# Performance work log

Hardware: AMD Instinct MI355X
Metric: run time of the kernel (lower is better)

Reference implementation:

```python
import jax, jax.numpy as jnp
import numpy as np
import math

B, C_IN, S, E, H, DFF = 8, 16, 1024, 128, 8, 512
DH = E // H
EPS_BN = 1e-5
EPS_LN = 1e-5


def _tape_pe(d_model, seq_len):
    pos = jnp.arange(seq_len, dtype=jnp.float32)[:, None]
    div = jnp.exp(jnp.arange(0, d_model, 2, dtype=jnp.float32) * (-math.log(10000.0) / d_model))
    ang = pos * div * (d_model / seq_len)
    pe = jnp.zeros((seq_len, d_model), dtype=jnp.float32)
    pe = pe.at[:, 0::2].set(jnp.sin(ang))
    pe = pe.at[:, 1::2].set(jnp.cos(ang))
    return pe  # [S, E]


def _ln(x, g, b, eps=EPS_LN):
    m = jnp.mean(x, axis=-1, keepdims=True)
    v = jnp.mean((x - m) ** 2, axis=-1, keepdims=True)
    return (x - m) / jnp.sqrt(v + eps) * g + b


def _bn(x, g, b, mean, var, eps=EPS_BN):
    # eval-mode BatchNorm2d over channel axis 1 of NCHW
    sh = (1, -1, 1, 1)
    return (x - mean.reshape(sh)) / jnp.sqrt(var.reshape(sh) + eps) * g.reshape(sh) + b.reshape(sh)


def setup_inputs() -> dict:
    key = jax.random.key(0)
    ks = jax.random.split(key, 24)
    f = lambda k, shape, s=0.05: (jax.random.normal(k, shape, dtype=jnp.float32) * s)
    inp = {
        'x': jax.random.normal(ks[0], (B, C_IN, S), dtype=jnp.float32),
        'conv1_w': f(ks[1], (E * 4, 1, 1, 7)),
        'conv1_b': f(ks[2], (E * 4,)),
        'bn1_g': 1.0 + f(ks[3], (E * 4,)),
        'bn1_b': f(ks[4], (E * 4,)),
        'bn1_m': jnp.zeros((E * 4,), jnp.float32),
        'bn1_v': jnp.ones((E * 4,), jnp.float32),
        'conv2_w': f(ks[5], (E, E * 4, C_IN, 1)),
        'conv2_b': f(ks[6], (E,)),
        'bn2_g': 1.0 + f(ks[7], (E,)),
        'bn2_b': f(ks[8], (E,)),
        'bn2_m': jnp.zeros((E,), jnp.float32),
        'bn2_v': jnp.ones((E,), jnp.float32),
        'wq': f(ks[9], (E, E)),
        'wk': f(ks[10], (E, E)),
        'wv': f(ks[11], (E, E)),
        'rel_bias_table': f(ks[12], (2 * S - 1, H), 0.02),
        'ln_attn_g': jnp.ones((E,), jnp.float32),
        'ln_attn_b': jnp.zeros((E,), jnp.float32),
        'ln1_g': jnp.ones((E,), jnp.float32),
        'ln1_b': jnp.zeros((E,), jnp.float32),
        'ln2_g': jnp.ones((E,), jnp.float32),
        'ln2_b': jnp.zeros((E,), jnp.float32),
        'ff_w1': f(ks[13], (DFF, E)),
        'ff_b1': f(ks[14], (DFF,)),
        'ff_w2': f(ks[15], (E, DFF)),
        'ff_b2': f(ks[16], (E,)),
    }
    return inp


def reference(x, conv1_w, conv1_b, bn1_g, bn1_b, bn1_m, bn1_v,
              conv2_w, conv2_b, bn2_g, bn2_b, bn2_m, bn2_v,
              wq, wk, wv, rel_bias_table,
              ln_attn_g, ln_attn_b, ln1_g, ln1_b, ln2_g, ln2_b,
              ff_w1, ff_b1, ff_w2, ff_b2):
    dn = ('NCHW', 'OIHW', 'NCHW')
    # conv stem: x [B, C_in, S] -> [B, 1, C_in, S]
    h = x[:, None, :, :]
    h = jax.lax.conv_general_dilated(h, conv1_w, (1, 1), [(0, 0), (3, 3)], dimension_numbers=dn)
    h = h + conv1_b[None, :, None, None]
    h = jax.nn.gelu(_bn(h, bn1_g, bn1_b, bn1_m, bn1_v), approximate=False)
    h = jax.lax.conv_general_dilated(h, conv2_w, (1, 1), [(0, 0), (0, 0)], dimension_numbers=dn)
    h = h + conv2_b[None, :, None, None]
    h = jax.nn.gelu(_bn(h, bn2_g, bn2_b, bn2_m, bn2_v), approximate=False)
    x_src = jnp.transpose(h[:, :, 0, :], (0, 2, 1))  # [B, S, E]

    # tAPE absolute positional encoding
    x_pos = x_src + _tape_pe(E, S)[None]

    # Attention_Rel_Scl (eRPE): bias added AFTER softmax, as in the original
    scale = E ** (-0.5)
    q = jnp.einsum('bsd,ed->bse', x_pos, wq).reshape(B, S, H, DH).transpose(0, 2, 1, 3)
    k = jnp.einsum('bsd,ed->bse', x_pos, wk).reshape(B, S, H, DH).transpose(0, 2, 1, 3)
    v = jnp.einsum('bsd,ed->bse', x_pos, wv).reshape(B, S, H, DH).transpose(0, 2, 1, 3)
    attn = jax.nn.softmax(jnp.einsum('bhid,bhjd->bhij', q, k) * scale, axis=-1)
    idx = jnp.arange(S)[:, None] - jnp.arange(S)[None, :] + (S - 1)  # [S, S]
    rel_bias = rel_bias_table[idx].transpose(2, 0, 1)[None]  # [1, H, S, S]
    attn = attn + rel_bias
    out = jnp.einsum('bhij,bhjd->bhid', attn, v).transpose(0, 2, 1, 3).reshape(B, S, E)
    out = _ln(out, ln_attn_g, ln_attn_b)

    att = _ln(x_src + out, ln1_g, ln1_b)
    ff = jnp.maximum(jnp.einsum('bsd,fd->bsf', att, ff_w1) + ff_b1, 0.0)
    ff = jnp.einsum('bsf,ef->bse', ff, ff_w2) + ff_b2
    y = _ln(att + ff, ln2_g, ln2_b)
    return jnp.transpose(y, (0, 2, 1))  # [B, E, S]
```

## Files before the change

### kernel.cpp

```cpp
#include <hip/hip_runtime.h>
#include <math.h>

#define BB    8
#define CIN   16
#define SS    1024
#define EE    128
#define HH    8
#define DHH   16
#define O1    512
#define DFFN  512
#define K2TOT 8192

#define PE_OFF    0
#define BN1SC_OFF 131072
#define BN1SH_OFF 131584
#define BN2SC_OFF 132096
#define BN2SH_OFF 132224
#define W1P_OFF   133120
#define WQKV_BF_OFF 135168
#define W1FF_BF_OFF 159744
#define W2FF_BF_OFF 192512
#define XSRC_OFF  262144
#define Q_OFF     1310720
#define KK_OFF    2359296
#define V_OFF     3407872
#define ATTN_OFF  4456448
#define ATT_OFF   5505024
#define FFH_OFF   6553600
#define W2CONV_BF_OFF 8650752

typedef __attribute__((ext_vector_type(8))) short short8;
typedef __attribute__((ext_vector_type(8))) unsigned short ushort8;
typedef __attribute__((ext_vector_type(4))) unsigned short us4;
typedef __attribute__((ext_vector_type(4))) float f32x4;
typedef _Float16 f16_t;
typedef __attribute__((ext_vector_type(4))) _Float16 half4;
typedef __attribute__((ext_vector_type(8))) _Float16 half8;

__device__ __forceinline__ float wave_sum(float v) {
    #pragma unroll
    for (int o = 32; o > 0; o >>= 1) v += __shfl_xor(v, o);
    return v;
}

__device__ __forceinline__ float gelu_exact(float x) {
    return 0.5f * x * (1.0f + erff(x * 0.7071067811865476f));
}

__device__ __forceinline__ float gelu_tanh(float x) {
    float x2 = x * x;
    float y = x * fmaf(0.0713548162f, x2, 1.5957691216f);
    float E = __expf(y);
    float r = __builtin_amdgcn_rcpf(E + 1.0f);
    return fmaf(-x, r, x);
}

__device__ __forceinline__ unsigned short f2bf(float f) {
    unsigned int u = __float_as_uint(f);
    unsigned int r = u + 0x7FFFu + ((u >> 16) & 1u);
    return (unsigned short)(r >> 16);
}

__device__ __forceinline__ float bf2f(unsigned short u) {
    return __uint_as_float(((unsigned int)u) << 16);
}

__device__ __forceinline__ void castw_body(const float* __restrict__ src,
                                           unsigned short* __restrict__ dst, int K, int tid) {
    int g = tid & 7, e = (tid >> 3) & 127, rest = tid >> 10;
    int KB = K >> 6;
    int kb = rest % KB, nb = rest / KB;
    int col = nb * 128 + e;
    const float* s = src + (size_t)col * K + kb * 64 + ((g ^ (e & 7)) << 3);
    ushort8 v;
    #pragma unroll
    for (int j = 0; j < 8; j++) v[j] = f2bf(s[j]);
    *(ushort8*)&dst[(size_t)tid << 3] = v;
}

__global__ __launch_bounds__(256) void k0_all(const float* __restrict__ conv1_w,
                                              const float* __restrict__ conv1_b,
                                              const float* __restrict__ bn1_g,
                                              const float* __restrict__ bn1_b,
                                              const float* __restrict__ bn1_m,
                                              const float* __restrict__ bn1_v,
                                              const float* __restrict__ conv2_w,
                                              const float* __restrict__ conv2_b,
                                              const float* __restrict__ bn2_g,
                                              const float* __restrict__ bn2_b,
                                              const float* __restrict__ bn2_m,
                                              const float* __restrict__ bn2_v,
                                              const float* __restrict__ wq,
                                              const float* __restrict__ wk,
                                              const float* __restrict__ wv,
                                              const float* __restrict__ ff_w1,
                                              const float* __restrict__ ff_w2,
                                              float* __restrict__ ws) {
    int bid = blockIdx.x, t = threadIdx.x;
    if (bid < 512) {
        int idx = bid * 256 + t;
        int s = idx >> 7, e = idx & 127;
        int i = e >> 1;
        float freq = expf((float)(2 * i) * (-9.210340371976184f / 128.0f));
        float ang = (float)s * freq * 0.125f;
        ws[PE_OFF + idx] = (e & 1) ? cosf(ang) : sinf(ang);
    } else if (bid < 515) {
        int u = (bid - 512) * 256 + t;
        if (u < 512) {
            float sc = bn1_g[u] * rsqrtf(bn1_v[u] + 1e-5f);
            ws[BN1SC_OFF + u] = sc;
            ws[BN1SH_OFF + u] = (conv1_b[u] - bn1_m[u]) * sc + bn1_b[u];
        } else if (u < 640) {
            int e = u - 512;
            float sc = bn2_g[e] * rsqrtf(bn2_v[e] + 1e-5f);
            ws[BN2SC_OFF + e] = sc;
            ws[BN2SH_OFF + e] = (conv2_b[e] - bn2_m[e]) * sc + bn2_b[e];
        }
    } else if (bid < 1027) {
        castw_body(conv2_w, (unsigned short*)(ws + W2CONV_BF_OFF), 8192, (bid - 515) * 256 + t);
    } else if (bid < 1035) {
        castw_body(wq, (unsigned short*)(ws + WQKV_BF_OFF), 128, (bid - 1027) * 256 + t);
    } else if (bid < 1043) {
        castw_body(wk, (unsigned short*)(ws + WQKV_BF_OFF) + 16384, 128, (bid - 1035) * 256 + t);
    } else if (bid < 1051) {
        castw_body(wv, (unsigned short*)(ws + WQKV_BF_OFF) + 32768, 128, (bid - 1043) * 256 + t);
    } else if (bid < 1083) {
        castw_body(ff_w1, (unsigned short*)(ws + W1FF_BF_OFF), 128, (bid - 1051) * 256 + t);
    } else if (bid < 1115) {
        castw_body(ff_w2, (unsigned short*)(ws + W2FF_BF_OFF), 512, (bid - 1083) * 256 + t);
    } else {
        unsigned short* w1p = (unsigned short*)(ws + W1P_OFF);
        for (int id = t; id < 4096; id += 256) {
            int o = id >> 3, u = id & 7;
            float sc = bn1_g[o] * rsqrtf(bn1_v[o] + 1e-5f);
            float v = (u < 7) ? conv1_w[o * 7 + u] * sc : 0.f;
            w1p[id] = f2bf(v);
        }
    }
}

__global__ __launch_bounds__(256) void k1_mfma(const float* __restrict__ x,
                                               float* __restrict__ ws) {
    __shared__ float xt[CIN][72];
    __shared__ unsigned short w1ps[128 * 8];
    __shared__ float sh1s[128];

    const int t = threadIdx.x;
    const int wave = t >> 6, lane = t & 63;
    const int row0 = blockIdx.x * 64;
    const int ksplit = blockIdx.y;
    const int b = row0 >> 10, s0 = row0 & 1023;
    const int obase = ksplit * 128;

    for (int i = t; i < CIN * 70; i += 256) {
        int c = i / 70, j = i % 70;
        int gs = s0 + j - 3;
        xt[c][j] = (gs >= 0 && gs < SS) ? x[(b * CIN + c) * SS + gs] : 0.f;
    }
    if (t < 128) {
        *(ushort8*)&w1ps[t << 3] =
            ((const ushort8*)((const unsigned short*)(ws + W1P_OFF)))[obase + t];
        sh1s[t] = ws[BN1SH_OFF + obase + t];
    }
    __syncthreads();

    const int lrow = lane & 15, lq = lane >> 4;
    const int srow_local = (wave << 4) + lrow;
    const int cbase = (lq & 1) << 3;

    float xv[56];
    #pragma unroll
    for (int c8 = 0; c8 < 8; ++c8)
        #pragma unroll
        for (int u = 0; u < 7; ++u)
            xv[c8 * 7 + u] = xt[cbase + c8][srow_local + u];

    int boff[16];
    #pragma unroll
    for (int ks2 = 0; ks2 < 2; ++ks2) {
        int G = (ks2 << 2) + lq;
        #pragma unroll
        for (int nf = 0; nf < 8; ++nf) {
            int e = (nf << 4) + lrow;
            boff[ks2 * 8 + nf] = (e << 7) + ((G ^ (e & 7)) << 4);
        }
    }

    const char* w2g = (const char*)(ws + W2CONV_BF_OFF);
    const int olq = lq >> 1;

    auto computeA = [&](int kbl, int ks2) -> short8 {
        int ol = (kbl << 2) + (ks2 << 1) + olq;
        ushort8 w8 = *(const ushort8*)&w1ps[ol << 3];
        float w0 = bf2f(w8[0]), w1_ = bf2f(w8[1]), w2_ = bf2f(w8[2]), w3 = bf2f(w8[3]);
        float w4 = bf2f(w8[4]), w5 = bf2f(w8[5]), w6 = bf2f(w8[6]);
        float sh = sh1s[ol];
        short8 a;
        #pragma unroll
        for (int j = 0; j < 8; ++j) {
            float p = xv[j*7]   * w0 + xv[j*7+1] * w1_ + xv[j*7+2] * w2_ + xv[j*7+3] * w3
                    + xv[j*7+4] * w4 + xv[j*7+5] * w5 + xv[j*7+6] * w6;
            a[j] = (short)f2bf(gelu_tanh(p + sh));
        }
        return a;
    };

    f32x4 acc[8];
    #pragma unroll
    for (int i = 0; i < 8; ++i) acc[i] = (f32x4){0.f, 0.f, 0.f, 0.f};

    #pragma unroll 1
    for (int kbl = 0; kbl < 32; ++kbl) {
        const char* g = w2g + ((size_t)((ksplit << 5) + kbl) << 14);
        short8 bA_[8];
        #pragma unroll
        for (int i = 0; i < 8; ++i) bA_[i] = *(const short8*)(g + boff[i]);
        short8 a0 = computeA(kbl, 0);
        short8 bB_[8];
        #pragma unroll
        for (int i = 0; i < 8; ++i) bB_[i] = *(const short8*)(g + boff[8 + i]);
        #pragma unroll
        for (int nf = 0; nf < 8; ++nf)
            acc[nf] = __builtin_amdgcn_mfma_f32_16x16x32_bf16(a0, bA_[nf], acc[nf], 0, 0, 0);
        short8 a1 = computeA(kbl, 1);
        #pragma unroll
        for (int nf = 0; nf < 8; ++nf)
            acc[nf] = __builtin_amdgcn_mfma_f32_16x16x32_bf16(a1, bB_[nf], acc[nf], 0, 0, 0);
    }

    float* P = ws + Q_OFF + (size_t)ksplit * 1048576;
    #pragma unroll
    for (int nf = 0; nf < 8; ++nf) {
        int e = (nf << 4) + lrow;
        #pragma unroll
        for (int r = 0; r < 4; ++r) {
            int srow = s0 + (wave << 4) + (lq << 2) + r;
            P[(((size_t)(b * SS + srow)) << 7) + e] = acc[nf][r];
        }
    }
}

__global__ __launch_bounds__(256) void k1b_combine(float* __restrict__ ws) {
    int f = (blockIdx.x * 256 + threadIdx.x) * 4;
    int e0 = f & 127;
    float4 p0 = *(const float4*)&ws[Q_OFF + f];
    float4 p1 = *(const float4*)&ws[KK_OFF + f];
    float4 p2 = *(const float4*)&ws[V_OFF + f];
    float4 p3 = *(const float4*)&ws[ATTN_OFF + f];
    float4 sc = *(const float4*)&ws[BN2SC_OFF + e0];
    float4 sh = *(const float4*)&ws[BN2SH_OFF + e0];
    float4 o;
    o.x = gelu_exact(fmaf((p0.x + p1.x) + (p2.x + p3.x), sc.x, sh.x));
    o.y = gelu_exact(fmaf((p0.y + p1.y) + (p2.y + p3.y), sc.y, sh.y));
    o.z = gelu_exact(fmaf((p0.z + p1.z) + (p2.z + p3.z), sc.z, sh.z));
    o.w = gelu_exact(fmaf((p0.w + p1.w) + (p2.w + p3.w), sc.w, sh.w));
    *(float4*)&ws[XSRC_OFF + f] = o;
}

__global__ __launch_bounds__(256) void k2_mfma(float* __restrict__ ws) {
    __shared__ unsigned short As[32 * 128];
    __shared__ unsigned short Bs[128 * 128];
    __shared__ float ys[32][132];
    const int t = threadIdx.x;
    const int rt = blockIdx.x, mat = blockIdx.y;
    const int wave = t >> 6, lane = t & 63;

    const char* bg = (const char*)((const unsigned short*)(ws + WQKV_BF_OFF) + mat * 16384);
    #pragma unroll
    for (int c8 = 0; c8 < 8; ++c8) {
        int off = c8 * 4096 + wave * 1024;
        __builtin_amdgcn_global_load_lds(
            (const __attribute__((address_space(1))) unsigned int*)(bg + off + lane * 16),
            (__attribute__((address_space(3))) unsigned int*)(&Bs[off >> 1]), 16, 0, 0);
    }
    const int bs0 = rt * 32;
    const int sl0 = bs0 & 1023;
    for (int i = t; i < 1024; i += 256) {
        int row = i >> 5, d0 = (i & 31) << 2;
        float4 xvv = *(const float4*)&ws[XSRC_OFF + (size_t)(bs0 + row) * EE + d0];
        float4 pv = *(const float4*)&ws[PE_OFF + (size_t)(sl0 + row) * EE + d0];
        us4 o;
        o[0] = f2bf(xvv.x + pv.x); o[1] = f2bf(xvv.y + pv.y);
        o[2] = f2bf(xvv.z + pv.z); o[3] = f2bf(xvv.w + pv.w);
        int slot = (d0 >> 3) ^ (row & 7);
        *(us4*)&As[(row << 7) + (slot << 3) + (d0 & 7)] = o;
    }
    __syncthreads();

    const int wr = wave >> 1, wc = wave & 1;
    const int lrow = lane & 15, lq = lane >> 4;
    f32x4 acc[4];
    #pragma unroll
    for (int i = 0; i < 4; i++) acc[i] = (f32x4){0.f, 0.f, 0.f, 0.f};

    #pragma unroll
    for (int ksname = 0; ksname < 4; ++ksname) {
        int G = (ksname << 2) + lq;
        int arow = (wr << 4) + lrow;
        short8 a = *(const short8*)&As[(arow << 7) + ((G ^ (arow & 7)) << 3)];
        #pragma unroll
        for (int nf = 0; nf < 4; ++nf) {
            int e = (wc << 6) + (nf << 4) + lrow;
            short8 bf = *(const short8*)&Bs[((G >> 3) << 13) + (e << 6) + (((G & 7) ^ (e & 7)) << 3)];
            acc[nf] = __builtin_amdgcn_mfma_f32_16x16x32_bf16(a, bf, acc[nf], 0, 0, 0);
        }
    }

    #pragma unroll
    for (int nf = 0; nf < 4; ++nf) {
        int e = (wc << 6) + (nf << 4) + lrow;
        #pragma unroll
        for (int r = 0; r < 4; ++r)
            ys[(wr << 4) + (lq << 2) + r][e] = acc[nf][r];
    }
    __syncthreads();

    const int b = bs0 >> 10;
    if (mat <= 1) {
        int row = t >> 3, h8 = t & 7;
        float scl = (mat == 0) ? 0.08838834764831845f : 1.0f;
        f16_t* dst = (f16_t*)(ws + (mat == 0 ? Q_OFF : KK_OFF))
                   + (((size_t)(b * HH + h8)) * SS + (sl0 + row)) * DHH;
        half8 v0, v1;
        #pragma unroll
        for (int d = 0; d < 8; d++) v0[d] = (f16_t)(ys[row][h8 * 16 + d] * scl);
        #pragma unroll
        for (int d = 0; d < 8; d++) v1[d] = (f16_t)(ys[row][h8 * 16 + 8 + d] * scl);
        *(half8*)&dst[0] = v0;
        *(half8*)&dst[8] = v1;
    } else {
        int c = t & 127, hf = t >> 7;
        int h8 = c >> 4, d2 = c & 15;
        f16_t* dst = (f16_t*)(ws + V_OFF)
                   + (((size_t)(b * HH + h8)) * DHH + d2) * SS + sl0 + hf * 16;
        half8 v0, v1;
        #pragma unroll
        for (int r = 0; r < 8; r++) v0[r] = (f16_t)ys[hf * 16 + r][c];
        #pragma unroll
        for (int r = 0; r < 8; r++) v1[r] = (f16_t)ys[hf * 16 + 8 + r][c];
        *(half8*)&dst[0] = v0;
        *(half8*)&dst[8] = v1;
    }
}

__global__ __launch_bounds__(256) void k3_attn(const float* __restrict__ rel_tab,
                                               float* __restrict__ ws) {
    __shared__ f16_t rtbl4[4][1088];
    const int bh = blockIdx.x;
    const int h = bh & 7, b = bh >> 3;
    const int i0b = blockIdx.y * 64;
    const int t = threadIdx.x;
    for (int id = t; id < 4 * 1088; id += 256) {
        int p = id / 1088; int j = id - p * 1088;
        int u = j + p;
        float v = (u < 1087) ? rel_tab[(i0b + 1086 - u) * HH + h] : 0.f;
        rtbl4[p][j] = (f16_t)v;
    }
    __syncthreads();

    const int w = t >> 6, lane = t & 63;
    const int q = lane & 15, g = lane >> 4;
    const int r = w * 16 + q;
    const int i = i0b + r;

    const f16_t* QH  = (const f16_t*)(ws + Q_OFF)  + (size_t)bh * SS * DHH;
    const f16_t* KH  = (const f16_t*)(ws + KK_OFF) + (size_t)bh * SS * DHH;
    const f16_t* VHT = (const f16_t*)(ws + V_OFF)  + (size_t)bh * DHH * SS;

    half4 qf = *(const half4*)&QH[(size_t)i * DHH + 4 * g];
    f32x4 o = {0.f, 0.f, 0.f, 0.f};
    f32x4 bv = {0.f, 0.f, 0.f, 0.f};
    const f32x4 zf = {0.f, 0.f, 0.f, 0.f};
    float lp = 0.f;
    const int p4 = (63 - r + 4 * g) & 3;

    #pragma unroll 4
    for (int jt = 0; jt < 64; ++jt) {
        half4 kf = *(const half4*)&KH[(size_t)(jt * 16 + q) * DHH + 4 * g];
        f32x4 s = __builtin_amdgcn_mfma_f32_16x16x16f16(kf, qf, zf, 0, 0, 0);
        float p0 = __expf(s[0]), p1 = __expf(s[1]), p2 = __expf(s[2]), p3 = __expf(s[3]);
        lp += (p0 + p1) + (p2 + p3);
        half4 pf;
        pf[0] = (f16_t)p0; pf[1] = (f16_t)p1; pf[2] = (f16_t)p2; pf[3] = (f16_t)p3;
        half4 vf = *(const half4*)&VHT[(size_t)q * SS + jt * 16 + 4 * g];
        o = __builtin_amdgcn_mfma_f32_16x16x16f16(vf, pf, o, 0, 0, 0);
        int vb = 63 - r + jt * 16 + 4 * g;
        half4 bfrag = *(const half4*)&rtbl4[p4][vb & ~3];
        bv = __builtin_amdgcn_mfma_f32_16x16x16f16(vf, bfrag, bv, 0, 0, 0);
    }
    lp += __shfl_xor(lp, 16);
    lp += __shfl_xor(lp, 32);
    float inv = 1.f / lp;
    float4 ov = make_float4(fmaf(o[0], inv, bv[0]), fmaf(o[1], inv, bv[1]),
                            fmaf(o[2], inv, bv[2]), fmaf(o[3], inv, bv[3]));
    *(float4*)&ws[ATTN_OFF + ((size_t)(b * SS) + i) * EE + h * DHH + 4 * g] = ov;
}

__global__ __launch_bounds__(256) void k4_ln(const float* __restrict__ g_attn, const float* __restrict__ b_attn,
                                             const float* __restrict__ g1, const float* __restrict__ b1,
                                             float* __restrict__ ws) {
    int row = blockIdx.x * 4 + (threadIdx.x >> 6);
    int lane = threadIdx.x & 63;
    int e0 = lane * 2;
    const float* ain = ws + ATTN_OFF + (size_t)row * EE;
    const float* xsr = ws + XSRC_OFF + (size_t)row * EE;
    float2 a = *(const float2*)(ain + e0);
    float mean = wave_sum(a.x + a.y) * (1.f / 128.f);
    float dx = a.x - mean, dy = a.y - mean;
    float var = wave_sum(dx * dx + dy * dy) * (1.f / 128.f);
    float inv = rsqrtf(var + 1e-5f);
    float n0 = dx * inv * g_attn[e0] + b_attn[e0];
    float n1 = dy * inv * g_attn[e0 + 1] + b_attn[e0 + 1];
    float2 xs2 = *(const float2*)(xsr + e0);
    float z0 = xs2.x + n0, z1 = xs2.y + n1;
    float m2 = wave_sum(z0 + z1) * (1.f / 128.f);
    float d0 = z0 - m2, d1 = z1 - m2;
    float v2 = wave_sum(d0 * d0 + d1 * d1) * (1.f / 128.f);
    float inv2 = rsqrtf(v2 + 1e-5f);
    float o0 = d0 * inv2 * g1[e0] + b1[e0];
    float o1 = d1 * inv2 * g1[e0 + 1] + b1[e0 + 1];
    *(float2*)(ws + ATT_OFF + (size_t)row * EE + e0) = make_float2(o0, o1);
}

__global__ __launch_bounds__(256) void k5_mfma(const float* __restrict__ b1,
                                               float* __restrict__ ws) {
    __shared__ unsigned short As[32 * 128];
    __shared__ unsigned short Bs[128 * 128];
    __shared__ float ys[32][132];
    const int t = threadIdx.x;
    const int rt = blockIdx.x, nb = blockIdx.y;
    const int wave = t >> 6, lane = t & 63;

    const char* bg = (const char*)((const unsigned short*)(ws + W1FF_BF_OFF) + nb * 16384);
    #pragma unroll
    for (int c8 = 0; c8 < 8; ++c8) {
        int off = c8 * 4096 + wave * 1024;
        __builtin_amdgcn_global_load_lds(
            (const __attribute__((address_space(1))) unsigned int*)(bg + off + lane * 16),
            (__attribute__((address_space(3))) unsigned int*)(&Bs[off >> 1]), 16, 0, 0);
    }
    const int bs0 = rt * 32;
    for (int i = t; i < 1024; i += 256) {
        int row = i >> 5, d0 = (i & 31) << 2;
        float4 xvv = *(const float4*)&ws[ATT_OFF + (size_t)(bs0 + row) * EE + d0];
        us4 o;
        o[0] = f2bf(xvv.x); o[1] = f2bf(xvv.y); o[2] = f2bf(xvv.z); o[3] = f2bf(xvv.w);
        int slot = (d0 >> 3) ^ (row & 7);
        *(us4*)&As[(row << 7) + (slot << 3) + (d0 & 7)] = o;
    }
    __syncthreads();

    const int wr = wave >> 1, wc = wave & 1;
    const int lrow = lane & 15, lq = lane >> 4;
    f32x4 acc[4];
    #pragma unroll
    for (int i = 0; i < 4; i++) acc[i] = (f32x4){0.f, 0.f, 0.f, 0.f};

    #pragma unroll
    for (int ksname = 0; ksname < 4; ++ksname) {
        int G = (ksname << 2) + lq;
        int arow = (wr << 4) + lrow;
        short8 a = *(const short8*)&As[(arow << 7) + ((G ^ (arow & 7)) << 3)];
        #pragma unroll
        for (int nf = 0; nf < 4; ++nf) {
            int e = (wc << 6) + (nf << 4) + lrow;
            short8 bf = *(const short8*)&Bs[((G >> 3) << 13) + (e << 6) + (((G & 7) ^ (e & 7)) << 3)];
            acc[nf] = __builtin_amdgcn_mfma_f32_16x16x32_bf16(a, bf, acc[nf], 0, 0, 0);
        }
    }

    #pragma unroll
    for (int nf = 0; nf < 4; ++nf) {
        int col = (wc << 6) + (nf << 4) + lrow;
        float bias = b1[(nb << 7) + col];
        #pragma unroll
        for (int r = 0; r < 4; ++r)
            ys[(wr << 4) + (lq << 2) + r][col] = fmaxf(acc[nf][r] + bias, 0.f);
    }
    __syncthreads();

    unsigned short* ffhb = (unsigned short*)(ws + FFH_OFF);
    #pragma unroll
    for (int kk = 0; kk < 2; ++kk) {
        int id = t + kk * 256;
        int ssr = id >> 4, fg = id & 15;
        float4 v0 = *(const float4*)&ys[ssr][fg * 8];
        float4 v1 = *(const float4*)&ys[ssr][fg * 8 + 4];
        ushort8 ov;
        ov[0] = f2bf(v0.x); ov[1] = f2bf(v0.y); ov[2] = f2bf(v0.z); ov[3] = f2bf(v0.w);
        ov[4] = f2bf(v1.x); ov[5] = f2bf(v1.y); ov[6] = f2bf(v1.z); ov[7] = f2bf(v1.w);
        int kb = (nb << 1) + (fg >> 3);
        int slot = (fg & 7) ^ (ssr & 7);
        *(ushort8*)&ffhb[(((size_t)(rt * 8 + kb) * 32 + ssr) << 6) + (slot << 3)] = ov;
    }
}

__global__ __launch_bounds__(256) void k6_mfma(const float* __restrict__ b2,
                                               const float* __restrict__ g2, const float* __restrict__ bb2,
                                               float* __restrict__ ws, float* __restrict__ out) {
    __shared__ unsigned short Ab[2][2048];
    __shared__ unsigned short Bb[2][8192];
    __shared__ float y[32][132];
    const int t = threadIdx.x;
    const int wave = t >> 6, lane = t & 63;
    const int rt = blockIdx.x;

    const char* ag = (const char*)((const unsigned short*)(ws + FFH_OFF) + (size_t)rt * 16384);
    const char* bgc = (const char*)(ws + W2FF_BF_OFF);

    auto stage = [&](int kb, int buf) {
        __builtin_amdgcn_global_load_lds(
            (const __attribute__((address_space(1))) unsigned int*)(ag + kb * 4096 + t * 16),
            (__attribute__((address_space(3))) unsigned int*)(&Ab[buf][(t * 16) >> 1]), 16, 0, 0);
        const char* g = bgc + kb * 16384;
        #pragma unroll
        for (int c4 = 0; c4 < 4; ++c4) {
            int off = c4 * 4096 + wave * 1024;
            __builtin_amdgcn_global_load_lds(
                (const __attribute__((address_space(1))) unsigned int*)(g + off + lane * 16),
                (__attribute__((address_space(3))) unsigned int*)(&Bb[buf][off >> 1]), 16, 0, 0);
        }
    };

    const int wr = wave >> 1, wc = wave & 1;
    const int lrow = lane & 15, lq = lane >> 4;
    f32x4 acc[4];
    #pragma unroll
    for (int i = 0; i < 4; i++) acc[i] = (f32x4){0.f, 0.f, 0.f, 0.f};

    stage(0, 0);
    __syncthreads();
    for (int kb = 0; kb < 8; ++kb) {
        int cur = kb & 1;
        if (kb < 7) stage(kb + 1, cur ^ 1);
        #pragma unroll
        for (int ksname = 0; ksname < 2; ++ksname) {
            int G = (ksname << 2) + lq;
            int arow = (wr << 4) + lrow;
            short8 a = *(const short8*)&Ab[cur][(arow << 6) + ((G ^ (arow & 7)) << 3)];
            #pragma unroll
            for (int nf = 0; nf < 4; ++nf) {
                int e = (wc << 6) + (nf << 4) + lrow;
                short8 bf = *(const short8*)&Bb[cur][(e << 6) + ((G ^ (e & 7)) << 3)];
                acc[nf] = __builtin_amdgcn_mfma_f32_16x16x32_bf16(a, bf, acc[nf], 0, 0, 0);
            }
        }
        __syncthreads();
    }

    const int bs0 = rt * 32;
    #pragma unroll
    for (int nf = 0; nf < 4; ++nf) {
        int e = (wc << 6) + (nf << 4) + lrow;
        float bvv = b2[e];
        #pragma unroll
        for (int r = 0; r < 4; ++r) {
            int row = (wr << 4) + (lq << 2) + r;
            y[row][e] = acc[nf][r] + bvv + ws[ATT_OFF + (size_t)(bs0 + row) * EE + e];
        }
    }
    __syncthreads();
    int e0 = lane * 2;
    for (int rr = 0; rr < 8; rr++) {
        int row = wave * 8 + rr;
        float z0 = y[row][e0], z1 = y[row][e0 + 1];
        float mean = wave_sum(z0 + z1) * (1.f / 128.f);
        float d0 = z0 - mean, d1 = z1 - mean;
        float var = wave_sum(d0 * d0 + d1 * d1) * (1.f / 128.f);
        float inv = rsqrtf(var + 1e-5f);
        y[row][e0]     = d0 * inv * g2[e0] + bb2[e0];
        y[row][e0 + 1] = d1 * inv * g2[e0 + 1] + bb2[e0 + 1];
    }
    __syncthreads();
    int b = bs0 >> 10, s0 = bs0 & 1023;
    int sl = t & 31, eg = t >> 5;
    #pragma unroll
    for (int rep = 0; rep < 16; rep++) {
        int e = eg * 16 + rep;
        out[(size_t)b * EE * SS + (size_t)e * SS + s0 + sl] = y[sl][e];
    }
}

extern "C" void kernel_launch(void* const* d_in, const int* in_sizes, int n_in,
                              void* d_out, int out_size, void* d_ws, size_t ws_size,
                              hipStream_t stream) {
    const float* x        = (const float*)d_in[0];
    const float* conv1_w  = (const float*)d_in[1];
    const float* conv1_b  = (const float*)d_in[2];
    const float* bn1_g    = (const float*)d_in[3];
    const float* bn1_b    = (const float*)d_in[4];
    const float* bn1_m    = (const float*)d_in[5];
    const float* bn1_v    = (const float*)d_in[6];
    const float* conv2_w  = (const float*)d_in[7];
    const float* conv2_b  = (const float*)d_in[8];
    const float* bn2_g    = (const float*)d_in[9];
    const float* bn2_b    = (const float*)d_in[10];
    const float* bn2_m    = (const float*)d_in[11];
    const float* bn2_v    = (const float*)d_in[12];
    const float* wq       = (const float*)d_in[13];
    const float* wk       = (const float*)d_in[14];
    const float* wv       = (const float*)d_in[15];
    const float* rel_tab  = (const float*)d_in[16];
    const float* ln_attn_g = (const float*)d_in[17];
    const float* ln_attn_b = (const float*)d_in[18];
    const float* ln1_g    = (const float*)d_in[19];
    const float* ln1_b    = (const float*)d_in[20];
    const float* ln2_g    = (const float*)d_in[21];
    const float* ln2_b    = (const float*)d_in[22];
    const float* ff_w1    = (const float*)d_in[23];
    const float* ff_b1    = (const float*)d_in[24];
    const float* ff_w2    = (const float*)d_in[25];
    const float* ff_b2    = (const float*)d_in[26];

    float* ws  = (float*)d_ws;
    float* out = (float*)d_out;

    hipLaunchKernelGGL(k0_all, dim3(1116), dim3(256), 0, stream,
                       conv1_w, conv1_b, bn1_g, bn1_b, bn1_m, bn1_v,
                       conv2_w, conv2_b, bn2_g, bn2_b, bn2_m, bn2_v,
                       wq, wk, wv, ff_w1, ff_w2, ws);
    hipLaunchKernelGGL(k1_mfma, dim3(128, 4), dim3(256), 0, stream, x, ws);
    hipLaunchKernelGGL(k1b_combine, dim3(1024), dim3(256), 0, stream, ws);
    hipLaunchKernelGGL(k2_mfma, dim3(256, 3), dim3(256), 0, stream, ws);
    hipLaunchKernelGGL(k3_attn, dim3(BB * HH, SS / 64), dim3(256), 0, stream, rel_tab, ws);
    hipLaunchKernelGGL(k4_ln, dim3(BB * SS / 4), dim3(256), 0, stream, ln_attn_g, ln_attn_b, ln1_g, ln1_b, ws);
    hipLaunchKernelGGL(k5_mfma, dim3(256, 4), dim3(256), 0, stream, ff_b1, ws);
    hipLaunchKernelGGL(k6_mfma, dim3(256), dim3(256), 0, stream, ff_b2, ln2_g, ln2_b, ws, out);
}
```

Before: 157.8 us.

## Reorder conv2 K dimension by channel and compute conv1 with fp16 dot2

The conv2 weight cast now reorders the reduction dimension so each K-split block handles 4 input channels across all 512 conv1 outputs, instead of 128 outputs across all 16 channels. The conv1 depthwise taps are computed with packed fp16 dot2 instructions, and the BN shift is folded in as an 8th weight against a constant 1. Blocks grow to 512 threads with a 4x2 wave tiling that halves the accumulators per wave. This cuts per-thread register pressure and conv1 FLOPs, at the cost of fp16 precision on x and the conv1 weights.

```diff
diff --git a/kernel.cpp b/kernel.cpp
--- a/kernel.cpp
+++ b/kernel.cpp
@@ -34,8 +34,21 @@
 typedef __attribute__((ext_vector_type(4))) unsigned short us4;
 typedef __attribute__((ext_vector_type(4))) float f32x4;
 typedef _Float16 f16_t;
+typedef __attribute__((ext_vector_type(2))) _Float16 half2t;
 typedef __attribute__((ext_vector_type(4))) _Float16 half4;
 typedef __attribute__((ext_vector_type(8))) _Float16 half8;
+
+#if defined(__has_builtin)
+#if __has_builtin(__builtin_amdgcn_fdot2)
+#define FDOT2(a, b, c) __builtin_amdgcn_fdot2((a), (b), (c), false)
+#endif
+#endif
+#ifndef FDOT2
+__device__ __forceinline__ float fdot2_fb(half2t a, half2t b, float c) {
+    return (float)a[0] * (float)b[0] + (float)a[1] * (float)b[1] + c;
+}
+#define FDOT2(a, b, c) fdot2_fb((a), (b), (c))
+#endif
 
 __device__ __forceinline__ float wave_sum(float v) {
     #pragma unroll
@@ -59,10 +72,6 @@
     unsigned int u = __float_as_uint(f);
     unsigned int r = u + 0x7FFFu + ((u >> 16) & 1u);
     return (unsigned short)(r >> 16);
-}
-
-__device__ __forceinline__ float bf2f(unsigned short u) {
-    return __uint_as_float(((unsigned int)u) << 16);
 }
 
 __device__ __forceinline__ void castw_body(const float* __restrict__ src,
@@ -117,7 +126,15 @@
             ws[BN2SH_OFF + e] = (conv2_b[e] - bn2_m[e]) * sc + bn2_b[e];
         }
     } else if (bid < 1027) {
-        castw_body(conv2_w, (unsigned short*)(ws + W2CONV_BF_OFF), 8192, (bid - 515) * 256 + t);
+        int tid = (bid - 515) * 256 + t;
+        int g = tid & 7, e = (tid >> 3) & 127, kb = tid >> 10;
+        int c = kb >> 3;
+        int obase = ((kb & 7) << 6) + ((g ^ (e & 7)) << 3);
+        const float* s = conv2_w + (size_t)e * K2TOT + obase * 16 + c;
+        ushort8 v;
+        #pragma unroll
+        for (int j = 0; j < 8; j++) v[j] = f2bf(s[j * 16]);
+        *(ushort8*)&((unsigned short*)(ws + W2CONV_BF_OFF))[(size_t)tid << 3] = v;
     } else if (bid < 1035) {
         castw_body(wq, (unsigned short*)(ws + WQKV_BF_OFF), 128, (bid - 1027) * 256 + t);
     } else if (bid < 1043) {
@@ -129,112 +146,120 @@
     } else if (bid < 1115) {
         castw_body(ff_w2, (unsigned short*)(ws + W2FF_BF_OFF), 512, (bid - 1083) * 256 + t);
     } else {
-        unsigned short* w1p = (unsigned short*)(ws + W1P_OFF);
+        f16_t* w1p = (f16_t*)(ws + W1P_OFF);
         for (int id = t; id < 4096; id += 256) {
             int o = id >> 3, u = id & 7;
             float sc = bn1_g[o] * rsqrtf(bn1_v[o] + 1e-5f);
-            float v = (u < 7) ? conv1_w[o * 7 + u] * sc : 0.f;
-            w1p[id] = f2bf(v);
-        }
-    }
-}
-
-__global__ __launch_bounds__(256) void k1_mfma(const float* __restrict__ x,
-                                               float* __restrict__ ws) {
-    __shared__ float xt[CIN][72];
-    __shared__ unsigned short w1ps[128 * 8];
-    __shared__ float sh1s[128];
+            float v;
+            if (u < 7)      v = conv1_w[o * 7 + u] * sc;
+            else            v = (conv1_b[o] - bn1_m[o]) * sc + bn1_b[o];
+            w1p[id] = (f16_t)v;
+        }
+    }
+}
+
+__global__ __launch_bounds__(512, 4) void k1_mfma(const float* __restrict__ x,
+                                                  float* __restrict__ ws) {
+    __shared__ float xt[4][72];
+    __shared__ unsigned int w1ps4[512 * 4];
 
     const int t = threadIdx.x;
     const int wave = t >> 6, lane = t & 63;
     const int row0 = blockIdx.x * 64;
     const int ksplit = blockIdx.y;
     const int b = row0 >> 10, s0 = row0 & 1023;
-    const int obase = ksplit * 128;
-
-    for (int i = t; i < CIN * 70; i += 256) {
-        int c = i / 70, j = i % 70;
+
+    for (int i = t; i < 4 * 70; i += 512) {
+        int cc = i / 70, j = i % 70;
         int gs = s0 + j - 3;
-        xt[c][j] = (gs >= 0 && gs < SS) ? x[(b * CIN + c) * SS + gs] : 0.f;
-    }
-    if (t < 128) {
-        *(ushort8*)&w1ps[t << 3] =
-            ((const ushort8*)((const unsigned short*)(ws + W1P_OFF)))[obase + t];
-        sh1s[t] = ws[BN1SH_OFF + obase + t];
-    }
-    __syncthreads();
-
+        xt[cc][j] = (gs >= 0 && gs < SS) ? x[(b * CIN + ksplit * 4 + cc) * SS + gs] : 0.f;
+    }
+    {
+        const uint4* w1pg = (const uint4*)(ws + W1P_OFF);
+        if (t < 512) ((uint4*)w1ps4)[t] = w1pg[t];
+    }
+    __syncthreads();
+
+    const int wr = wave >> 1, wc = wave & 1;
     const int lrow = lane & 15, lq = lane >> 4;
-    const int srow_local = (wave << 4) + lrow;
-    const int cbase = (lq & 1) << 3;
-
-    float xv[56];
-    #pragma unroll
-    for (int c8 = 0; c8 < 8; ++c8)
-        #pragma unroll
-        for (int u = 0; u < 7; ++u)
-            xv[c8 * 7 + u] = xt[cbase + c8][srow_local + u];
-
-    int boff[16];
+    const int srow_local = (wr << 4) + lrow;
+
+    half2t xx[4][4];
+    #pragma unroll
+    for (int cc = 0; cc < 4; ++cc) {
+        float a0 = xt[cc][srow_local], a1 = xt[cc][srow_local + 1];
+        float a2 = xt[cc][srow_local + 2], a3 = xt[cc][srow_local + 3];
+        float a4 = xt[cc][srow_local + 4], a5 = xt[cc][srow_local + 5];
+        float a6 = xt[cc][srow_local + 6];
+        xx[cc][0][0] = (f16_t)a0; xx[cc][0][1] = (f16_t)a1;
+        xx[cc][1][0] = (f16_t)a2; xx[cc][1][1] = (f16_t)a3;
+        xx[cc][2][0] = (f16_t)a4; xx[cc][2][1] = (f16_t)a5;
+        xx[cc][3][0] = (f16_t)a6; xx[cc][3][1] = (f16_t)1.0f;
+    }
+
+    int boff[8];
     #pragma unroll
     for (int ks2 = 0; ks2 < 2; ++ks2) {
         int G = (ks2 << 2) + lq;
         #pragma unroll
-        for (int nf = 0; nf < 8; ++nf) {
-            int e = (nf << 4) + lrow;
-            boff[ks2 * 8 + nf] = (e << 7) + ((G ^ (e & 7)) << 4);
+        for (int nf = 0; nf < 4; ++nf) {
+            int e = (wc << 6) + (nf << 4) + lrow;
+            boff[ks2 * 4 + nf] = (e << 7) + ((G ^ (e & 7)) << 4);
         }
     }
 
     const char* w2g = (const char*)(ws + W2CONV_BF_OFF);
-    const int olq = lq >> 1;
-
-    auto computeA = [&](int kbl, int ks2) -> short8 {
-        int ol = (kbl << 2) + (ks2 << 1) + olq;
-        ushort8 w8 = *(const ushort8*)&w1ps[ol << 3];
-        float w0 = bf2f(w8[0]), w1_ = bf2f(w8[1]), w2_ = bf2f(w8[2]), w3 = bf2f(w8[3]);
-        float w4 = bf2f(w8[4]), w5 = bf2f(w8[5]), w6 = bf2f(w8[6]);
-        float sh = sh1s[ol];
+
+    auto computeA = [&](half2t x0, half2t x1, half2t x2, half2t x3, int obase) -> short8 {
         short8 a;
         #pragma unroll
         for (int j = 0; j < 8; ++j) {
-            float p = xv[j*7]   * w0 + xv[j*7+1] * w1_ + xv[j*7+2] * w2_ + xv[j*7+3] * w3
-                    + xv[j*7+4] * w4 + xv[j*7+5] * w5 + xv[j*7+6] * w6;
-            a[j] = (short)f2bf(gelu_tanh(p + sh));
+            uint4 w = *(const uint4*)&w1ps4[(obase + j) << 2];
+            float p = FDOT2(__builtin_bit_cast(half2t, w.x), x0,
+                      FDOT2(__builtin_bit_cast(half2t, w.y), x1,
+                      FDOT2(__builtin_bit_cast(half2t, w.z), x2,
+                      FDOT2(__builtin_bit_cast(half2t, w.w), x3, 0.0f))));
+            a[j] = (short)f2bf(gelu_tanh(p));
         }
         return a;
     };
 
-    f32x4 acc[8];
-    #pragma unroll
-    for (int i = 0; i < 8; ++i) acc[i] = (f32x4){0.f, 0.f, 0.f, 0.f};
-
-    #pragma unroll 1
-    for (int kbl = 0; kbl < 32; ++kbl) {
-        const char* g = w2g + ((size_t)((ksplit << 5) + kbl) << 14);
-        short8 bA_[8];
-        #pragma unroll
-        for (int i = 0; i < 8; ++i) bA_[i] = *(const short8*)(g + boff[i]);
-        short8 a0 = computeA(kbl, 0);
-        short8 bB_[8];
-        #pragma unroll
-        for (int i = 0; i < 8; ++i) bB_[i] = *(const short8*)(g + boff[8 + i]);
-        #pragma unroll
-        for (int nf = 0; nf < 8; ++nf)
-            acc[nf] = __builtin_amdgcn_mfma_f32_16x16x32_bf16(a0, bA_[nf], acc[nf], 0, 0, 0);
-        short8 a1 = computeA(kbl, 1);
-        #pragma unroll
-        for (int nf = 0; nf < 8; ++nf)
-            acc[nf] = __builtin_amdgcn_mfma_f32_16x16x32_bf16(a1, bB_[nf], acc[nf], 0, 0, 0);
+    f32x4 acc[4];
+    #pragma unroll
+    for (int i = 0; i < 4; ++i) acc[i] = (f32x4){0.f, 0.f, 0.f, 0.f};
+
+    #pragma unroll
+    for (int cg = 0; cg < 4; ++cg) {
+        half2t x0 = xx[cg][0], x1 = xx[cg][1], x2 = xx[cg][2], x3 = xx[cg][3];
+        #pragma unroll 1
+        for (int k8 = 0; k8 < 8; ++k8) {
+            int kbg = (ksplit << 5) + (cg << 3) + k8;
+            const char* g = w2g + ((size_t)kbg << 14);
+            int ob = (k8 << 6) + (lq << 3);
+            short8 bA_[4];
+            #pragma unroll
+            for (int i = 0; i < 4; ++i) bA_[i] = *(const short8*)(g + boff[i]);
+            short8 a0 = computeA(x0, x1, x2, x3, ob);
+            short8 bB_[4];
+            #pragma unroll
+            for (int i = 0; i < 4; ++i) bB_[i] = *(const short8*)(g + boff[4 + i]);
+            #pragma unroll
+            for (int nf = 0; nf < 4; ++nf)
+                acc[nf] = __builtin_amdgcn_mfma_f32_16x16x32_bf16(a0, bA_[nf], acc[nf], 0, 0, 0);
+            short8 a1 = computeA(x0, x1, x2, x3, ob + 32);
+            #pragma unroll
+            for (int nf = 0; nf < 4; ++nf)
+                acc[nf] = __builtin_amdgcn_mfma_f32_16x16x32_bf16(a1, bB_[nf], acc[nf], 0, 0, 0);
+        }
     }
 
     float* P = ws + Q_OFF + (size_t)ksplit * 1048576;
     #pragma unroll
-    for (int nf = 0; nf < 8; ++nf) {
-        int e = (nf << 4) + lrow;
+    for (int nf = 0; nf < 4; ++nf) {
+        int e = (wc << 6) + (nf << 4) + lrow;
         #pragma unroll
         for (int r = 0; r < 4; ++r) {
-            int srow = s0 + (wave << 4) + (lq << 2) + r;
+            int srow = s0 + (wr << 4) + (lq << 2) + r;
             P[(((size_t)(b * SS + srow)) << 7) + e] = acc[nf][r];
         }
     }
@@ -619,7 +644,7 @@
                        conv1_w, conv1_b, bn1_g, bn1_b, bn1_m, bn1_v,
                        conv2_w, conv2_b, bn2_g, bn2_b, bn2_m, bn2_v,
                        wq, wk, wv, ff_w1, ff_w2, ws);
-    hipLaunchKernelGGL(k1_mfma, dim3(128, 4), dim3(256), 0, stream, x, ws);
+    hipLaunchKernelGGL(k1_mfma, dim3(128, 4), dim3(512), 0, stream, x, ws);
     hipLaunchKernelGGL(k1b_combine, dim3(1024), dim3(256), 0, stream, ws);
     hipLaunchKernelGGL(k2_mfma, dim3(256, 3), dim3(256), 0, stream, ws);
     hipLaunchKernelGGL(k3_attn, dim3(BB * HH, SS / 64), dim3(256), 0, stream, rel_tab, ws);
```

Result: slower. 185.6 us (+17.6%).

## Permute conv2 weight layout so each lane computes A fragments for two channels

Applied to the files above, without the earlier changes.

Changes the bf16 layout of the conv2 weights so the MFMA k-dimension interleaves two conv1 output channels with four input channels per lane, instead of one channel with eight input channels. Each lane now holds 28 x values instead of 56 and computes two channels' 7-tap convolutions over four input channels. This cuts register pressure and the per-lane x loads, at the cost of reading two weight vectors and two shifts per fragment. The total conv1 plus GELU arithmetic per lane is unchanged. The B-fragment offsets are simplified to one table, with an XOR used for the second k-slice.

```diff
diff --git a/kernel.cpp b/kernel.cpp
--- a/kernel.cpp
+++ b/kernel.cpp
@@ -117,7 +117,17 @@
             ws[BN2SH_OFF + e] = (conv2_b[e] - bn2_m[e]) * sc + bn2_b[e];
         }
     } else if (bid < 1027) {
-        castw_body(conv2_w, (unsigned short*)(ws + W2CONV_BF_OFF), 8192, (bid - 515) * 256 + t);
+        int tid = (bid - 515) * 256 + t;
+        int g = tid & 7, e = (tid >> 3) & 127, kb = tid >> 10;
+        int gg = g ^ (e & 7);
+        int o0 = (kb << 2) + ((gg >> 2) << 1);
+        int c0 = (gg & 3) << 2;
+        const float* s = conv2_w + (size_t)e * K2TOT;
+        ushort8 v;
+        #pragma unroll
+        for (int j = 0; j < 8; j++)
+            v[j] = f2bf(s[(o0 + (j & 1)) * 16 + c0 + (j >> 1)]);
+        *(ushort8*)&((unsigned short*)(ws + W2CONV_BF_OFF))[(size_t)tid << 3] = v;
     } else if (bid < 1035) {
         castw_body(wq, (unsigned short*)(ws + WQKV_BF_OFF), 128, (bid - 1027) * 256 + t);
     } else if (bid < 1043) {
@@ -166,41 +176,41 @@
 
     const int lrow = lane & 15, lq = lane >> 4;
     const int srow_local = (wave << 4) + lrow;
-    const int cbase = (lq & 1) << 3;
-
-    float xv[56];
-    #pragma unroll
-    for (int c8 = 0; c8 < 8; ++c8)
+    const int cbase = lq << 2;
+
+    float xv[28];
+    #pragma unroll
+    for (int c4 = 0; c4 < 4; ++c4)
         #pragma unroll
         for (int u = 0; u < 7; ++u)
-            xv[c8 * 7 + u] = xt[cbase + c8][srow_local + u];
-
-    int boff[16];
-    #pragma unroll
-    for (int ks2 = 0; ks2 < 2; ++ks2) {
-        int G = (ks2 << 2) + lq;
-        #pragma unroll
-        for (int nf = 0; nf < 8; ++nf) {
-            int e = (nf << 4) + lrow;
-            boff[ks2 * 8 + nf] = (e << 7) + ((G ^ (e & 7)) << 4);
-        }
+            xv[c4 * 7 + u] = xt[cbase + c4][srow_local + u];
+
+    int boff[8];
+    #pragma unroll
+    for (int nf = 0; nf < 8; ++nf) {
+        int e = (nf << 4) + lrow;
+        boff[nf] = (e << 7) + ((lq ^ (e & 7)) << 4);
     }
 
     const char* w2g = (const char*)(ws + W2CONV_BF_OFF);
-    const int olq = lq >> 1;
 
     auto computeA = [&](int kbl, int ks2) -> short8 {
-        int ol = (kbl << 2) + (ks2 << 1) + olq;
-        ushort8 w8 = *(const ushort8*)&w1ps[ol << 3];
-        float w0 = bf2f(w8[0]), w1_ = bf2f(w8[1]), w2_ = bf2f(w8[2]), w3 = bf2f(w8[3]);
-        float w4 = bf2f(w8[4]), w5 = bf2f(w8[5]), w6 = bf2f(w8[6]);
-        float sh = sh1s[ol];
+        int o0 = (kbl << 2) + (ks2 << 1);
+        ushort8 wa = *(const ushort8*)&w1ps[o0 << 3];
+        ushort8 wb = *(const ushort8*)&w1ps[(o0 + 1) << 3];
+        float sha = sh1s[o0], shb = sh1s[o0 + 1];
         short8 a;
         #pragma unroll
-        for (int j = 0; j < 8; ++j) {
-            float p = xv[j*7]   * w0 + xv[j*7+1] * w1_ + xv[j*7+2] * w2_ + xv[j*7+3] * w3
-                    + xv[j*7+4] * w4 + xv[j*7+5] * w5 + xv[j*7+6] * w6;
-            a[j] = (short)f2bf(gelu_tanh(p + sh));
+        for (int jh = 0; jh < 4; ++jh) {
+            const float* xp = &xv[jh * 7];
+            float pe = xp[0]*bf2f(wa[0]) + xp[1]*bf2f(wa[1]) + xp[2]*bf2f(wa[2])
+                     + xp[3]*bf2f(wa[3]) + xp[4]*bf2f(wa[4]) + xp[5]*bf2f(wa[5])
+                     + xp[6]*bf2f(wa[6]);
+            float po = xp[0]*bf2f(wb[0]) + xp[1]*bf2f(wb[1]) + xp[2]*bf2f(wb[2])
+                     + xp[3]*bf2f(wb[3]) + xp[4]*bf2f(wb[4]) + xp[5]*bf2f(wb[5])
+                     + xp[6]*bf2f(wb[6]);
+            a[2 * jh]     = (short)f2bf(gelu_tanh(pe + sha));
+            a[2 * jh + 1] = (short)f2bf(gelu_tanh(po + shb));
         }
         return a;
     };
@@ -218,7 +228,7 @@
         short8 a0 = computeA(kbl, 0);
         short8 bB_[8];
         #pragma unroll
-        for (int i = 0; i < 8; ++i) bB_[i] = *(const short8*)(g + boff[8 + i]);
+        for (int i = 0; i < 8; ++i) bB_[i] = *(const short8*)(g + (boff[i] ^ 64));
         #pragma unroll
         for (int nf = 0; nf < 8; ++nf)
             acc[nf] = __builtin_amdgcn_mfma_f32_16x16x32_bf16(a0, bA_[nf], acc[nf], 0, 0, 0);
```

After: 159.8 us. Within noise of the previous version (+1.2%).
